# Kernel optimization log

Measured on AMD Instinct MI355X. Metric: run time of the kernel, lower is better.

## Reference

```python
import jax, jax.numpy as jnp
import numpy as np

B, S, E, H, FF = 4, 2048, 512, 8, 2048
DH = E // H
EPS = 1e-6


def setup_inputs() -> dict:
    key = jax.random.key(0)
    ks = jax.random.split(key, 16)
    sc = lambda fan_in: 1.0 / np.sqrt(fan_in)
    inp = {
        "x": jax.random.normal(ks[0], (B, S, E), dtype=jnp.float32),
        "src_mask": jnp.ones((B, 1, 1, S), dtype=jnp.int32),
        # attention projections, stored [in, out]
        "wq": jax.random.uniform(ks[1], (E, E), minval=-sc(E), maxval=sc(E)),
        "bq": jnp.zeros((E,), jnp.float32),
        "wk": jax.random.uniform(ks[2], (E, E), minval=-sc(E), maxval=sc(E)),
        "bk": jnp.zeros((E,), jnp.float32),
        "wv": jax.random.uniform(ks[3], (E, E), minval=-sc(E), maxval=sc(E)),
        "bv": jnp.zeros((E,), jnp.float32),
        "wo": jax.random.uniform(ks[4], (E, E), minval=-sc(E), maxval=sc(E)),
        "bo": jnp.zeros((E,), jnp.float32),
        # feed-forward
        "w1": jax.random.uniform(ks[5], (E, FF), minval=-sc(E), maxval=sc(E)),
        "b1": jnp.zeros((FF,), jnp.float32),
        "w2": jax.random.uniform(ks[6], (FF, E), minval=-sc(FF), maxval=sc(FF)),
        "b2": jnp.zeros((E,), jnp.float32),
        # addNormLayer scalar params (alpha init 1, bias init 0)
        "alpha1": jnp.ones((1,), jnp.float32),
        "beta1": jnp.zeros((1,), jnp.float32),
        "alpha2": jnp.ones((1,), jnp.float32),
        "beta2": jnp.zeros((1,), jnp.float32),
    }
    return inp


def _norm(x, alpha, beta):
    # matches torch: mean + unbiased std (ddof=1), eps added to std
    mean = jnp.mean(x, axis=-1, keepdims=True)
    std = jnp.std(x, axis=-1, keepdims=True, ddof=1)
    return alpha * (x - mean) / (std + EPS) + beta


def reference(x, src_mask, wq, bq, wk, bk, wv, bv, wo, bo,
              w1, b1, w2, b2, alpha1, beta1, alpha2, beta2):
    # --- residual 1: pre-norm self-attention ---
    n = _norm(x, alpha1, beta1)  # [B,S,E]
    q = (n @ wq + bq).reshape(B, S, H, DH).transpose(0, 2, 1, 3)  # [B,H,S,DH]
    k = (n @ wk + bk).reshape(B, S, H, DH).transpose(0, 2, 1, 3)
    v = (n @ wv + bv).reshape(B, S, H, DH).transpose(0, 2, 1, 3)
    scores = jnp.einsum('bhqd,bhkd->bhqk', q, k) / np.sqrt(DH)  # [B,H,S,S]
    scores = jnp.where(src_mask == 0, -1e9, scores)
    attn = jax.nn.softmax(scores, axis=-1)
    ctx = jnp.einsum('bhqk,bhkd->bhqd', attn, v)  # [B,H,S,DH]
    ctx = ctx.transpose(0, 2, 1, 3).reshape(B, S, E)
    x = x + (ctx @ wo + bo)
    # --- residual 2: pre-norm FFN ---
    n2 = _norm(x, alpha2, beta2)
    ff = jax.nn.relu(n2 @ w1 + b1) @ w2 + b2
    return x + ff
```

## Files before the change

### kernel.cpp

```cpp
#include <hip/hip_runtime.h>
#include <type_traits>

typedef __bf16 bfrag __attribute__((ext_vector_type(8)));
typedef float f32x4 __attribute__((ext_vector_type(4)));
typedef float f32x16 __attribute__((ext_vector_type(16)));
typedef unsigned short us8 __attribute__((ext_vector_type(8)));
typedef unsigned int u32x2 __attribute__((ext_vector_type(2)));
typedef unsigned int u32x4 __attribute__((ext_vector_type(4)));

__device__ __forceinline__ float bf2f(unsigned short s) {
  unsigned u = ((unsigned)s) << 16;
  float f;
  __builtin_memcpy(&f, &u, 4);
  return f;
}
__device__ __forceinline__ unsigned short f2bf(float f) {
  unsigned u;
  __builtin_memcpy(&u, &f, 4);
  u += 0x7fffu + ((u >> 16) & 1u);
  return (unsigned short)(u >> 16);
}
__device__ __forceinline__ float rdf(const void* p, size_t i, int isf) {
  return isf ? ((const float*)p)[i] : bf2f(((const unsigned short*)p)[i]);
}
__device__ __forceinline__ void gld16(const unsigned short* g, unsigned short* l) {
  __builtin_amdgcn_global_load_lds(
      (const __attribute__((address_space(1))) unsigned int*)g,
      (__attribute__((address_space(3))) unsigned int*)l, 16, 0, 0);
}
__device__ __forceinline__ unsigned cvtpk_bf16(float a, float b) {
  unsigned d;
  asm("v_cvt_pk_bf16_f32 %0, %1, %2" : "=v"(d) : "v"(a), "v"(b));
  return d;
}

template <int XMODE>
__device__ void norm_unit(const void* xin, const void* alpha, const void* beta,
                          unsigned short* out, int isf, int u) {
  constexpr int E = 512;
  int xf = XMODE ? 1 : isf;
  int tid = threadIdx.x;
  int wave = tid >> 6, lane = tid & 63;
  size_t tok = (size_t)u * 4 + wave;
  float v[8];
  if (xf) {
    const float* xp = (const float*)xin + tok * E + lane * 8;
    float4 a0 = *(const float4*)xp;
    float4 a1 = *(const float4*)(xp + 4);
    v[0] = a0.x; v[1] = a0.y; v[2] = a0.z; v[3] = a0.w;
    v[4] = a1.x; v[5] = a1.y; v[6] = a1.z; v[7] = a1.w;
  } else {
    us8 uu = *(const us8*)((const unsigned short*)xin + tok * E + lane * 8);
#pragma unroll
    for (int j = 0; j < 8; j++) v[j] = bf2f(uu[j]);
  }
  float s = 0.f, sq = 0.f;
#pragma unroll
  for (int j = 0; j < 8; j++) { s += v[j]; sq += v[j] * v[j]; }
#pragma unroll
  for (int off = 1; off < 64; off <<= 1) {
    s += __shfl_xor(s, off, 64);
    sq += __shfl_xor(sq, off, 64);
  }
  float mean = s * (1.0f / 512.0f);
  float var = fmaxf((sq - 512.0f * mean * mean) * (1.0f / 511.0f), 0.0f);
  float inv = rdf(alpha, 0, isf) / (sqrtf(var) + 1e-6f);
  float be = rdf(beta, 0, isf);
  us8 ov;
#pragma unroll
  for (int j = 0; j < 8; j++) ov[j] = f2bf((v[j] - mean) * inv + be);
  *(us8*)(out + tok * E + lane * 8) = ov;
}

__global__ __launch_bounds__(256) void setup_k(
    const unsigned short* __restrict__ x16,
    const void* wq, const void* wk, const void* wv, const void* wo,
    const void* w1, const void* w2,
    unsigned short* wqkvT, unsigned short* woT,
    unsigned short* w1T, unsigned short* w2T,
    const void* bq, const void* bk, const void* bv, const void* bo,
    const void* b1, const void* b2, float* __restrict__ bcat,
    const void* alpha1, const void* beta1, unsigned short* __restrict__ n1,
    int* __restrict__ flag) {
  __shared__ unsigned short tile[32][33];
  __shared__ int s_cnt;
  int tid = threadIdx.x;
  int bid = blockIdx.x;
  if (tid == 0) s_cnt = 0;
  __syncthreads();
  {
    int c = 0;
    for (int i = tid; i < 4096; i += 256) {
      unsigned short s = x16[2 * i];
      int e = (s >> 7) & 0xFF;
      if (e > 0xC2 || (e != 0 && e < 0x3D)) c++;
    }
    atomicAdd(&s_cnt, c);
  }
  __syncthreads();
  const int isf = (s_cnt > 256) ? 1 : 0;
  if (bid == 0 && tid == 0) flag[0] = isf;

  if (bid >= 3090) {
    norm_unit<0>(x16, alpha1, beta1, n1, isf, bid - 3090);
    return;
  }
  if (bid >= 3072) {
    int i = (bid - 3072) * 256 + tid;
    if (i < 4608) {
      float v;
      if (i < 512) v = rdf(bq, i, isf);
      else if (i < 1024) v = rdf(bk, i - 512, isf);
      else if (i < 1536) v = rdf(bv, i - 1024, isf);
      else if (i < 2048) v = rdf(bo, i - 1536, isf);
      else if (i < 4096) v = rdf(b1, i - 2048, isf);
      else v = rdf(b2, i - 4096, isf);
      bcat[i] = v;
    }
    return;
  }
  const void* W;
  unsigned short* Wt;
  int K, N, t;
  if (bid < 1024) {
    K = 512; N = 512; t = bid & 255;
    if (bid < 256) { W = wq; Wt = wqkvT; }
    else if (bid < 512) { W = wk; Wt = wqkvT + 262144; }
    else if (bid < 768) { W = wv; Wt = wqkvT + 524288; }
    else { W = wo; Wt = woT; }
  } else if (bid < 2048) {
    W = w1; Wt = w1T; K = 512; N = 2048; t = bid - 1024;
  } else {
    W = w2; Wt = w2T; K = 2048; N = 512; t = bid - 2048;
  }
  int nx = N >> 5;
  int n0 = (t % nx) * 32, k0 = (t / nx) * 32;
#pragma unroll
  for (int i = 0; i < 4; i++) {
    int e = tid + i * 256;
    int r = e >> 5, c = e & 31;
    tile[r][c] = f2bf(rdf(W, (size_t)(k0 + r) * N + n0 + c, isf));
  }
  __syncthreads();
#pragma unroll
  for (int i = 0; i < 4; i++) {
    int e = tid + i * 256;
    int r = e >> 5, c = e & 31;
    Wt[(size_t)(n0 + r) * K + k0 + c] = tile[c][r];
  }
}

__global__ __launch_bounds__(256) void vtrans_k(
    const unsigned short* __restrict__ qkb, unsigned short* __restrict__ vbt) {
  __shared__ unsigned short tile[32][33];
  int tid = threadIdx.x;
  int u = blockIdx.x;
  int s0 = (u & 63) * 32;
  int d0 = ((u >> 6) & 1) * 32;
  int bh = u >> 7, b = bh >> 3, h = bh & 7;
#pragma unroll
  for (int i = 0; i < 4; i++) {
    int e = tid + i * 256;
    int r = e >> 5, c = e & 31;
    tile[r][c] = qkb[((size_t)b * 2048 + s0 + r) * 1536 + 1024 + h * 64 + d0 + c];
  }
  __syncthreads();
#pragma unroll
  for (int i = 0; i < 4; i++) {
    int e = tid + i * 256;
    int r = e >> 5, c = e & 31;
    vbt[((size_t)bh * 64 + d0 + r) * 2048 + s0 + c] = tile[c][r];
  }
}

__global__ __launch_bounds__(256) void norm2_k(
    const void* __restrict__ xin, const void* __restrict__ alpha,
    const void* __restrict__ beta, unsigned short* __restrict__ out,
    const int* __restrict__ flag) {
  norm_unit<1>(xin, alpha, beta, out, flag[0], blockIdx.x);
}

template <int TN, int RES, int OUTM, int RELU, int QSC>
__global__ __launch_bounds__(256, 3) void gemm2_k(
    const unsigned short* __restrict__ A,
    const unsigned short* __restrict__ Bt,
    const float* __restrict__ bias,
    const void* __restrict__ res,
    void* __restrict__ outp,
    int N, int K, const int* __restrict__ flag) {
  constexpr int MT = (TN == 128) ? 4 : 2;
  constexpr int BROWS = TN / 4;
  __shared__ alignas(16) unsigned short As[128 * 64];
  __shared__ alignas(16) unsigned short Bs[TN * 64];
  int isf = flag[0];
  int outf32 = (OUTM == 1) || (OUTM == 2 && isf);
  int tid = threadIdx.x;
  int wave = tid >> 6, lane = tid & 63;
  int quad = lane >> 4, l16 = lane & 15, l7 = l16 & 7;
  int wm = (TN == 128) ? (wave >> 1) : wave;
  int wn = (TN == 128) ? (wave & 1) : 0;
  size_t m0 = (size_t)blockIdx.x * 128;
  size_t n0 = (size_t)blockIdx.y * TN;

  int lrow = lane >> 3;
  int gcol = 8 * ((lane & 7) ^ lrow);

  const unsigned short* ag = A + (m0 + wave * 32 + lrow) * K + gcol;
  const unsigned short* bg = Bt + (n0 + wave * BROWS + lrow) * K + gcol;
  unsigned short* asl = &As[(wave * 32) * 64];
  unsigned short* bsl = &Bs[(wave * BROWS) * 64];

  f32x4 acc[MT][4];
#pragma unroll
  for (int i = 0; i < MT; i++)
#pragma unroll
    for (int j = 0; j < 4; j++) acc[i][j] = {0.f, 0.f, 0.f, 0.f};

  for (int k0 = 0; k0 < K; k0 += 64) {
    __syncthreads();
#pragma unroll
    for (int c = 0; c < 4; c++)
      gld16(ag + (size_t)(8 * c) * K + k0, asl + (8 * c) * 64);
#pragma unroll
    for (int c = 0; c < BROWS / 8; c++)
      gld16(bg + (size_t)(8 * c) * K + k0, bsl + (8 * c) * 64);
    __syncthreads();
#pragma unroll
    for (int ko = 0; ko < 2; ko++) {
      int slot = ((4 * ko + quad) ^ l7) * 8;
      bfrag af[MT], bf[4];
#pragma unroll
      for (int i = 0; i < MT; i++)
        af[i] = *(const bfrag*)&As[(wm * (MT * 16) + i * 16 + l16) * 64 + slot];
#pragma unroll
      for (int j = 0; j < 4; j++)
        bf[j] = *(const bfrag*)&Bs[(wn * 64 + j * 16 + l16) * 64 + slot];
#pragma unroll
      for (int i = 0; i < MT; i++)
#pragma unroll
        for (int j = 0; j < 4; j++)
          acc[i][j] = __builtin_amdgcn_mfma_f32_16x16x32_bf16(af[i], bf[j], acc[i][j], 0, 0, 0);
    }
  }
#pragma unroll
  for (int j = 0; j < 4; j++) {
    size_t n = n0 + wn * 64 + j * 16 + l16;
    float bv = bias[n];
#pragma unroll
    for (int i = 0; i < MT; i++) {
#pragma unroll
      for (int r = 0; r < 4; r++) {
        size_t m = m0 + wm * (MT * 16) + i * 16 + quad * 4 + r;
        float vv = acc[i][j][r] + bv;
        if (QSC && n < 512) vv *= 0.18033688f;
        if (RELU) vv = fmaxf(vv, 0.0f);
        if (RES == 1) vv += rdf(res, m * N + n, isf);
        else if (RES == 2) vv += ((const float*)res)[m * N + n];
        if (outf32) ((float*)outp)[m * N + n] = vv;
        else ((unsigned short*)outp)[m * N + n] = f2bf(vv);
      }
    }
  }
}

__global__ __launch_bounds__(512) void attn_k(
    const unsigned short* __restrict__ qkb,
    const unsigned short* __restrict__ vbt,
    const int* __restrict__ mask,
    unsigned short* __restrict__ ctx) {
  constexpr int S = 2048;
  __shared__ alignas(16) unsigned short Kt[2][2][64 * 64];
  __shared__ alignas(16) unsigned short Vt[2][2][64 * 64];
  __shared__ alignas(16) float mskf[S];
  __shared__ float ml[2][256];
  __shared__ int s_all;
  int tid = threadIdx.x, wave = tid >> 6, lane = tid & 63;
  int kh = wave >> 2, wv = wave & 3;
  int l32 = lane & 31, hi = lane >> 5;

  int lin = blockIdx.x;
  int work = (lin & 7) * 32 + (lin >> 3);
  int bh = work >> 3;
  int q0 = (work & 7) * 256;
  int b = bh >> 3, h = bh & 7;
  size_t rowbase = (size_t)b * S;

  bfrag qf[2][4];
#pragma unroll
  for (int qg = 0; qg < 2; qg++) {
    const unsigned short* qp =
        qkb + (rowbase + q0 + wv * 64 + qg * 32 + l32) * 1536 + h * 64 + hi * 8;
#pragma unroll
    for (int ds = 0; ds < 4; ds++) qf[qg][ds] = *(const bfrag*)(qp + ds * 16);
  }

  int srow_l = lane >> 3;
  int sc = lane & 7;
  int swz = (sc ^ srow_l) * 8;
  const unsigned short* kgb = qkb + 512 + h * 64;
  const unsigned short* vgb = vbt + (size_t)bh * 64 * S;

  const unsigned short* kp[2];
  const unsigned short* vp[2];
#pragma unroll
  for (int i = 0; i < 2; i++) {
    int r = wv * 16 + i * 8 + srow_l;
    kp[i] = kgb + (rowbase + kh * 1024 + r) * 1536 + swz;
    vp[i] = vgb + (size_t)r * S + kh * 1024 + swz;
  }

  auto STAGE = [&](int buf) {
#pragma unroll
    for (int i = 0; i < 2; i++) {
      gld16(kp[i], &Kt[kh][buf][(wv * 16 + i * 8) * 64]);
      kp[i] += 64 * 1536;
      gld16(vp[i], &Vt[kh][buf][(wv * 16 + i * 8) * 64]);
      vp[i] += 64;
    }
  };

  f32x16 o[4];
#pragma unroll
  for (int i = 0; i < 4; i++)
#pragma unroll
    for (int j = 0; j < 16; j++) o[i][j] = 0.f;
  float l_i[2] = {0.f, 0.f};

  STAGE(0);
  if (tid == 0) s_all = 1;
  __syncthreads();
  {
    int ok = 1;
    for (int i = tid; i < S; i += 512) {
      int mv = mask[rowbase + i];
      ok &= (mv != 0);
      mskf[i] = mv ? 0.0f : -1e5f;
    }
    atomicAnd(&s_all, ok);
  }
  __syncthreads();
  int am = s_all;

  auto BODY = [&](auto amc) {
    constexpr bool AM = decltype(amc)::value;
    for (int it = 0; it < 16; it++) {
      int cur = it & 1;
      if (it + 1 < 16) STAGE(cur ^ 1);

#pragma unroll
      for (int qg = 0; qg < 2; qg++) {
#pragma unroll
        for (int t = 0; t < 2; t++) {
          f32x16 pacc;
          {
            int r = t * 32 + l32;
            f32x16 z = {};
#pragma unroll
            for (int ds = 0; ds < 4; ds++) {
              int phys = ((2 * ds + hi) ^ (l32 & 7)) * 8;
              bfrag kf = *(const bfrag*)&Kt[kh][cur][r * 64 + phys];
              pacc = __builtin_amdgcn_mfma_f32_32x32x16_bf16(
                  kf, qf[qg][ds], ds == 0 ? z : pacc, 0, 0, 0);
            }
          }
          unsigned pb[8];
#pragma unroll
          for (int g = 0; g < 4; g++) {
            float p0, p1, p2, p3;
            if constexpr (AM) {
              p0 = __builtin_amdgcn_exp2f(pacc[g * 4 + 0]);
              p1 = __builtin_amdgcn_exp2f(pacc[g * 4 + 1]);
              p2 = __builtin_amdgcn_exp2f(pacc[g * 4 + 2]);
              p3 = __builtin_amdgcn_exp2f(pacc[g * 4 + 3]);
            } else {
              float4 m4 =
                  *(const float4*)&mskf[kh * 1024 + it * 64 + t * 32 + g * 8 + hi * 4];
              p0 = __builtin_amdgcn_exp2f(pacc[g * 4 + 0] + m4.x);
              p1 = __builtin_amdgcn_exp2f(pacc[g * 4 + 1] + m4.y);
              p2 = __builtin_amdgcn_exp2f(pacc[g * 4 + 2] + m4.z);
              p3 = __builtin_amdgcn_exp2f(pacc[g * 4 + 3] + m4.w);
            }
            l_i[qg] += (p0 + p1) + (p2 + p3);
            pb[g * 2] = cvtpk_bf16(p0, p1);
            pb[g * 2 + 1] = cvtpk_bf16(p2, p3);
          }
#pragma unroll
          for (int e = 0; e < 2; e++) {
            u32x2 sA = __builtin_amdgcn_permlane32_swap(
                pb[4 * e + 0], pb[4 * e + 2], false, false);
            u32x2 sB = __builtin_amdgcn_permlane32_swap(
                pb[4 * e + 1], pb[4 * e + 3], false, false);
            u32x4 pw = {sA.x, sB.x, sA.y, sB.y};
            bfrag pf = __builtin_bit_cast(bfrag, pw);
            int ks = 2 * t + e;
#pragma unroll
            for (int dt = 0; dt < 2; dt++) {
              int r = dt * 32 + l32;
              int phys = ((2 * ks + hi) ^ (l32 & 7)) * 8;
              bfrag vf = *(const bfrag*)&Vt[kh][cur][r * 64 + phys];
              o[qg * 2 + dt] = __builtin_amdgcn_mfma_f32_32x32x16_bf16(
                  pf, vf, o[qg * 2 + dt], 0, 0, 0);
            }
          }
        }
      }
      __syncthreads();
    }
  };
  if (am) BODY(std::integral_constant<bool, true>{});
  else    BODY(std::integral_constant<bool, false>{});

#pragma unroll
  for (int qg = 0; qg < 2; qg++) {
    unsigned lu = __builtin_bit_cast(unsigned, l_i[qg]);
    u32x2 lr = __builtin_amdgcn_permlane32_swap(lu, lu, false, false);
    float l_tot = __builtin_bit_cast(float, lr.x) + __builtin_bit_cast(float, lr.y);
    if (lane < 32) ml[kh][wv * 64 + qg * 32 + l32] = l_tot;
  }
  float* mrgK = (float*)&Kt[0][0][0];
  float* mrgV = (float*)&Vt[0][0][0];
  if (kh == 1) {
#pragma unroll
    for (int qg = 0; qg < 2; qg++) {
#pragma unroll
      for (int reg = 0; reg < 16; reg++) {
        int ql = (reg & 3) + 8 * (reg >> 2) + 4 * hi;
        int qi = wv * 64 + qg * 32 + ql;
        mrgK[qi * 32 + l32] = o[qg * 2 + 0][reg];
        mrgV[qi * 32 + l32] = o[qg * 2 + 1][reg];
      }
    }
  }
  __syncthreads();
  if (kh == 0) {
#pragma unroll
    for (int qg = 0; qg < 2; qg++) {
#pragma unroll
      for (int reg = 0; reg < 16; reg++) {
        int ql = (reg & 3) + 8 * (reg >> 2) + 4 * hi;
        int qi = wv * 64 + qg * 32 + ql;
        float inv = 1.0f / fmaxf(ml[0][qi] + ml[1][qi], 1e-30f);
        size_t qrow = rowbase + q0 + qi;
        float v0 = (o[qg * 2 + 0][reg] + mrgK[qi * 32 + l32]) * inv;
        float v1 = (o[qg * 2 + 1][reg] + mrgV[qi * 32 + l32]) * inv;
        ctx[qrow * 512 + h * 64 + l32] = f2bf(v0);
        ctx[qrow * 512 + h * 64 + 32 + l32] = f2bf(v1);
      }
    }
  }
}

extern "C" void kernel_launch(void* const* d_in, const int* in_sizes, int n_in,
                              void* d_out, int out_size, void* d_ws, size_t ws_size,
                              hipStream_t stream) {
  const unsigned short* x = (const unsigned short*)d_in[0];
  const int* mask         = (const int*)d_in[1];
  const void* wq = d_in[2];  const void* bq = d_in[3];
  const void* wk = d_in[4];  const void* bk = d_in[5];
  const void* wv = d_in[6];  const void* bv = d_in[7];
  const void* wo = d_in[8];  const void* bo = d_in[9];
  const void* w1 = d_in[10]; const void* b1 = d_in[11];
  const void* w2 = d_in[12]; const void* b2 = d_in[13];
  const void* alpha1 = d_in[14]; const void* beta1 = d_in[15];
  const void* alpha2 = d_in[16]; const void* beta2 = d_in[17];

  char* ws = (char*)d_ws;
  int* flag            = (int*)(ws + 0);
  unsigned short* wqkvT= (unsigned short*)(ws + 65536);
  unsigned short* woT  = (unsigned short*)(ws + 1638400);
  unsigned short* w1T  = (unsigned short*)(ws + 2162688);
  unsigned short* w2T  = (unsigned short*)(ws + 4259840);
  float*          bcat = (float*)         (ws + 6356992);
  float*          x1   = (float*)         (ws + 6422528);
  unsigned short* n1   = (unsigned short*)(ws + 23199744);
  unsigned short* qkb  = (unsigned short*)(ws + 31588352);
  unsigned short* vbt  = (unsigned short*)(ws + 56754176);
  unsigned short* ff1  = qkb;

  dim3 blk(256);

  setup_k<<<5138, blk, 0, stream>>>(x, wq, wk, wv, wo, w1, w2,
                                    wqkvT, woT, w1T, w2T,
                                    bq, bk, bv, bo, b1, b2, bcat,
                                    alpha1, beta1, n1, flag);
  gemm2_k<128, 0, 0, 0, 1><<<dim3(64, 12), blk, 0, stream>>>(n1, wqkvT, bcat, nullptr, qkb, 1536, 512, flag);
  vtrans_k<<<4096, blk, 0, stream>>>(qkb, vbt);
  attn_k<<<256, dim3(512), 0, stream>>>(qkb, vbt, mask, n1);
  gemm2_k<64, 1, 1, 0, 0><<<dim3(64, 8), blk, 0, stream>>>(n1, woT, bcat + 1536, (const void*)x, x1, 512, 512, flag);
  norm2_k<<<2048, blk, 0, stream>>>(x1, alpha2, beta2, n1, flag);
  gemm2_k<128, 0, 0, 1, 0><<<dim3(64, 16), blk, 0, stream>>>(n1, w1T, bcat + 2048, nullptr, ff1, 2048, 512, flag);
  gemm2_k<64, 2, 2, 0, 0><<<dim3(64, 8), blk, 0, stream>>>(ff1, w2T, bcat + 4096, x1, d_out, 512, 2048, flag);
}
```

Before: 265.0 us.

## Fuse V transpose into QKV GEMM epilogue and remap blocks for XCD locality

Removes the separate V-transpose kernel by having the QKV GEMM write the V columns directly in transposed [b,h,d,s] layout with 4-element packed stores. It also remaps linear block indices so that blocks landing on the same XCD share B-tiles, aiming for better L2 reuse. This saves one launch and a full read/write pass over V. In exchange the transposed stores are strided, with 8-byte writes per lane.

```diff
diff --git a/kernel.cpp b/kernel.cpp
--- a/kernel.cpp
+++ b/kernel.cpp
@@ -5,6 +5,7 @@
 typedef float f32x4 __attribute__((ext_vector_type(4)));
 typedef float f32x16 __attribute__((ext_vector_type(16)));
 typedef unsigned short us8 __attribute__((ext_vector_type(8)));
+typedef unsigned short us4 __attribute__((ext_vector_type(4)));
 typedef unsigned int u32x2 __attribute__((ext_vector_type(2)));
 typedef unsigned int u32x4 __attribute__((ext_vector_type(4)));
 
@@ -150,29 +151,6 @@
   }
 }
 
-__global__ __launch_bounds__(256) void vtrans_k(
-    const unsigned short* __restrict__ qkb, unsigned short* __restrict__ vbt) {
-  __shared__ unsigned short tile[32][33];
-  int tid = threadIdx.x;
-  int u = blockIdx.x;
-  int s0 = (u & 63) * 32;
-  int d0 = ((u >> 6) & 1) * 32;
-  int bh = u >> 7, b = bh >> 3, h = bh & 7;
-#pragma unroll
-  for (int i = 0; i < 4; i++) {
-    int e = tid + i * 256;
-    int r = e >> 5, c = e & 31;
-    tile[r][c] = qkb[((size_t)b * 2048 + s0 + r) * 1536 + 1024 + h * 64 + d0 + c];
-  }
-  __syncthreads();
-#pragma unroll
-  for (int i = 0; i < 4; i++) {
-    int e = tid + i * 256;
-    int r = e >> 5, c = e & 31;
-    vbt[((size_t)bh * 64 + d0 + r) * 2048 + s0 + c] = tile[c][r];
-  }
-}
-
 __global__ __launch_bounds__(256) void norm2_k(
     const void* __restrict__ xin, const void* __restrict__ alpha,
     const void* __restrict__ beta, unsigned short* __restrict__ out,
@@ -180,13 +158,14 @@
   norm_unit<1>(xin, alpha, beta, out, flag[0], blockIdx.x);
 }
 
-template <int TN, int RES, int OUTM, int RELU, int QSC>
+template <int TN, int RES, int OUTM, int RELU, int QSC, int VT>
 __global__ __launch_bounds__(256, 3) void gemm2_k(
     const unsigned short* __restrict__ A,
     const unsigned short* __restrict__ Bt,
     const float* __restrict__ bias,
     const void* __restrict__ res,
     void* __restrict__ outp,
+    unsigned short* __restrict__ vbt,
     int N, int K, const int* __restrict__ flag) {
   constexpr int MT = (TN == 128) ? 4 : 2;
   constexpr int BROWS = TN / 4;
@@ -199,8 +178,11 @@
   int quad = lane >> 4, l16 = lane & 15, l7 = l16 & 7;
   int wm = (TN == 128) ? (wave >> 1) : wave;
   int wn = (TN == 128) ? (wave & 1) : 0;
-  size_t m0 = (size_t)blockIdx.x * 128;
-  size_t n0 = (size_t)blockIdx.y * TN;
+
+  int lin = (int)blockIdx.x + 64 * (int)blockIdx.y;
+  int xcd = lin & 7, kk = lin >> 3;
+  size_t m0 = (size_t)(xcd * 8 + (kk & 7)) * 128;
+  size_t n0 = (size_t)(kk >> 3) * TN;
 
   int lrow = lane >> 3;
   int gcol = 8 * ((lane & 7) ^ lrow);
@@ -241,6 +223,25 @@
         for (int j = 0; j < 4; j++)
           acc[i][j] = __builtin_amdgcn_mfma_f32_16x16x32_bf16(af[i], bf[j], acc[i][j], 0, 0, 0);
     }
+  }
+  if (VT && n0 >= 1024) {
+    int bq = (int)(m0 >> 11);
+    int sbase = (int)(m0 & 2047) + wm * (MT * 16) + quad * 4;
+#pragma unroll
+    for (int j = 0; j < 4; j++) {
+      int n = (int)n0 + wn * 64 + j * 16 + l16;
+      float bv = bias[n];
+      int hh = (n - 1024) >> 6, d = (n - 1024) & 63;
+      size_t row = ((size_t)(bq * 8 + hh) * 64 + d) * 2048;
+#pragma unroll
+      for (int i = 0; i < MT; i++) {
+        us4 pk;
+#pragma unroll
+        for (int r = 0; r < 4; r++) pk[r] = f2bf(acc[i][j][r] + bv);
+        *(us4*)&vbt[row + sbase + i * 16] = pk;
+      }
+    }
+    return;
   }
 #pragma unroll
   for (int j = 0; j < 4; j++) {
@@ -483,11 +484,10 @@
                                     wqkvT, woT, w1T, w2T,
                                     bq, bk, bv, bo, b1, b2, bcat,
                                     alpha1, beta1, n1, flag);
-  gemm2_k<128, 0, 0, 0, 1><<<dim3(64, 12), blk, 0, stream>>>(n1, wqkvT, bcat, nullptr, qkb, 1536, 512, flag);
-  vtrans_k<<<4096, blk, 0, stream>>>(qkb, vbt);
+  gemm2_k<128, 0, 0, 0, 1, 1><<<dim3(64, 12), blk, 0, stream>>>(n1, wqkvT, bcat, nullptr, qkb, vbt, 1536, 512, flag);
   attn_k<<<256, dim3(512), 0, stream>>>(qkb, vbt, mask, n1);
-  gemm2_k<64, 1, 1, 0, 0><<<dim3(64, 8), blk, 0, stream>>>(n1, woT, bcat + 1536, (const void*)x, x1, 512, 512, flag);
+  gemm2_k<64, 1, 1, 0, 0, 0><<<dim3(64, 8), blk, 0, stream>>>(n1, woT, bcat + 1536, (const void*)x, x1, nullptr, 512, 512, flag);
   norm2_k<<<2048, blk, 0, stream>>>(x1, alpha2, beta2, n1, flag);
-  gemm2_k<128, 0, 0, 1, 0><<<dim3(64, 16), blk, 0, stream>>>(n1, w1T, bcat + 2048, nullptr, ff1, 2048, 512, flag);
-  gemm2_k<64, 2, 2, 0, 0><<<dim3(64, 8), blk, 0, stream>>>(ff1, w2T, bcat + 4096, x1, d_out, 512, 2048, flag);
-}
+  gemm2_k<128, 0, 0, 1, 0, 0><<<dim3(64, 16), blk, 0, stream>>>(n1, w1T, bcat + 2048, nullptr, ff1, nullptr, 2048, 512, flag);
+  gemm2_k<64, 2, 2, 0, 0, 0><<<dim3(64, 8), blk, 0, stream>>>(ff1, w2T, bcat + 4096, x1, d_out, nullptr, 512, 2048, flag);
+}
```

Result: no change. 267.3 us (+0.9%).
